# Kernel tuning notes

Measured on AMD Instinct MI355X. Metric: run time of the kernel, lower is better.

The kernel has to match this reference:

```python
import jax, jax.numpy as jnp
import numpy as np

N = 50000      # nodes
E = 600000     # edges (avg degree 12)
IN = 128       # in_feat
HID = IN // 2  # 64
OUT = 128      # out_feat (must equal in_feat, see msg_linear)

# NOTE: the torch source uses nn.LeakyReLU(True): the positional arg is
# negative_slope, so slope == 1.0 (identity). We reproduce that faithfully.
NEG_SLOPE = 1.0

def leaky(v):
    return jnp.where(v >= 0, v, NEG_SLOPE * v)

def _linear_params(key, fan_in, fan_out):
    kw, kb = jax.random.split(key)
    bound = 1.0 / np.sqrt(fan_in)
    W = jax.random.uniform(kw, (fan_in, fan_out), jnp.float32, -bound, bound)
    b = jax.random.uniform(kb, (fan_out,), jnp.float32, -bound, bound)
    return W, b

def setup_inputs() -> dict:
    key = jax.random.key(0)
    ks = jax.random.split(key, 10)
    x = jax.random.normal(ks[0], (N, IN), jnp.float32)
    e = jax.random.normal(ks[1], (E, IN), jnp.float32)
    src = jax.random.randint(ks[2], (E,), 0, N, jnp.int64)
    dst = jax.random.randint(ks[3], (E,), 0, N, jnp.int64)
    W_nl1, b_nl1 = _linear_params(ks[4], IN, HID)    # node_linear1
    W_el, b_el = _linear_params(ks[5], IN, HID)      # edge_linear
    W1, b1 = _linear_params(ks[6], HID, HID)         # node_mlp layer 1
    W2, b2 = _linear_params(ks[7], HID, OUT)         # node_mlp layer 2
    W_nl2, b_nl2 = _linear_params(ks[8], IN, HID)    # node_linear2
    km, ke = jax.random.split(ks[9])
    W_ml, b_ml = _linear_params(km, IN, HID)         # msg_linear (in_feat==out_feat)
    W_em, b_em = _linear_params(ke, HID, OUT)        # edge_mlp layer
    return dict(x=x, e=e, src=src, dst=dst,
                W_nl1=W_nl1, b_nl1=b_nl1, W_el=W_el, b_el=b_el,
                W1=W1, b1=b1, W2=W2, b2=b2,
                W_nl2=W_nl2, b_nl2=b_nl2, W_ml=W_ml, b_ml=b_ml,
                W_em=W_em, b_em=b_em)

def reference(x, e, src, dst,
              W_nl1, b_nl1, W_el, b_el,
              W1, b1, W2, b2,
              W_nl2, b_nl2, W_ml, b_ml,
              W_em, b_em):
    # apply_edges: e' = node_mlp(node_linear1(x[src]) + edge_linear(e))
    z = x[src] @ W_nl1 + b_nl1 + e @ W_el + b_el            # [E, HID]
    e_new = leaky(leaky(z) @ W1 + b1) @ W2 + b2             # [E, OUT]
    # update_all(copy_e, sum): scatter-sum edge messages to destination nodes
    msg = jax.ops.segment_sum(e_new, dst, num_segments=N)   # [N, OUT]
    # x' = edge_mlp(node_linear2(x) + msg_linear(msg))
    h = leaky(x @ W_nl2 + b_nl2 + msg @ W_ml + b_ml)        # [N, HID]
    return h @ W_em + b_em                                  # [N, OUT]
```

## Files before the change

kernel.cpp:

```cpp
#include <hip/hip_runtime.h>

#define N_NODES 50000
#define N_EDGES 600000

#define WF_XS   0
#define WF_ES   6400000
#define WI_CNT   12800000
#define WI_OFF   12850000
#define WI_CUR   12900000
#define WI_BSUM  12950000
#define WI_BOFF  12950256
#define WI_EPAIR 12950512
#define WF_U    14160000
#define WF_V    14168192
#define WF_G    14184576
#define WF_P    14192768
#define WF_Q    14209152
#define WF_C1   14225536
#define WF_BE   14241920
#define WF_R    14242048
#define WF_C2   14242176

#define NBLK_SCAN 196

__global__ void pre1_kernel(const float* __restrict__ W1, const float* __restrict__ W2,
                            const float* __restrict__ b1, const float* __restrict__ b2,
                            const float* __restrict__ W_ml, const float* __restrict__ W_em,
                            const float* __restrict__ W_nl2, const float* __restrict__ b_nl2,
                            const float* __restrict__ b_ml, const float* __restrict__ b_em,
                            float* __restrict__ U, float* __restrict__ V,
                            float* __restrict__ C1, float* __restrict__ be,
                            float* __restrict__ c2) {
    int idx = blockIdx.x * 256 + threadIdx.x;
    if (idx < 8192) {
        int i = idx >> 7, j = idx & 127;
        float s = 0.f;
        for (int k = 0; k < 64; ++k) s += W1[i*64+k] * W2[k*128+j];
        U[idx] = s;
    } else if (idx < 24576) {
        int t = idx - 8192; int i = t >> 7, j = t & 127;
        float s = 0.f;
        for (int k = 0; k < 64; ++k) s += W_ml[i*64+k] * W_em[k*128+j];
        V[t] = s;
    } else if (idx < 40960) {
        int t = idx - 24576; int i = t >> 7, j = t & 127;
        float s = 0.f;
        for (int k = 0; k < 64; ++k) s += W_nl2[i*64+k] * W_em[k*128+j];
        C1[t] = s;
    } else if (idx < 41088) {
        int j = idx - 40960;
        float s = b2[j];
        for (int k = 0; k < 64; ++k) s += b1[k] * W2[k*128+j];
        be[j] = s;
    } else if (idx < 41216) {
        int j = idx - 41088;
        float s = b_em[j];
        for (int k = 0; k < 64; ++k) s += (b_nl2[k] + b_ml[k]) * W_em[k*128+j];
        c2[j] = s;
    }
}

__global__ void pre2_kernel(const float* __restrict__ U, const float* __restrict__ V,
                            float* __restrict__ G) {
    int idx = blockIdx.x * 256 + threadIdx.x;
    if (idx >= 8192) return;
    int i = idx >> 7, j = idx & 127;
    float s = 0.f;
    for (int k = 0; k < 128; ++k) s += U[i*128+k] * V[k*128+j];
    G[idx] = s;
}

__global__ void pre3_kernel(const float* __restrict__ W_nl1, const float* __restrict__ W_el,
                            const float* __restrict__ b_nl1, const float* __restrict__ b_el,
                            const float* __restrict__ G, const float* __restrict__ V,
                            const float* __restrict__ be,
                            float* __restrict__ P, float* __restrict__ Q,
                            float* __restrict__ r) {
    int idx = blockIdx.x * 256 + threadIdx.x;
    if (idx < 16384) {
        int i = idx >> 7, j = idx & 127;
        float s = 0.f;
        for (int k = 0; k < 64; ++k) s += W_nl1[i*64+k] * G[k*128+j];
        P[idx] = s;
    } else if (idx < 32768) {
        int t = idx - 16384; int i = t >> 7, j = t & 127;
        float s = 0.f;
        for (int k = 0; k < 64; ++k) s += W_el[i*64+k] * G[k*128+j];
        Q[t] = s;
    } else if (idx < 32896) {
        int j = idx - 32768;
        float s = 0.f;
        for (int k = 0; k < 64; ++k)  s += (b_nl1[k] + b_el[k]) * G[k*128+j];
        for (int k = 0; k < 128; ++k) s += be[k] * V[k*128+j];
        r[j] = s;
    }
}

__global__ __launch_bounds__(256) void zero_kernel(int* __restrict__ cnt) {
    int i = blockIdx.x * 256 + threadIdx.x;
    if (i < N_NODES) cnt[i] = 0;
}

__global__ __launch_bounds__(256) void hist_kernel(const int* __restrict__ dst,
                                                   int* __restrict__ cnt) {
    int e = blockIdx.x * 256 + threadIdx.x;
    if (e < N_EDGES) atomicAdd(&cnt[dst[e]], 1);
}

__global__ __launch_bounds__(256) void scan_a_kernel(const int* __restrict__ cnt,
                                                     int* __restrict__ bsum) {
    __shared__ int s[256];
    int i = blockIdx.x * 256 + threadIdx.x;
    int v = (i < N_NODES) ? cnt[i] : 0;
    s[threadIdx.x] = v;
    __syncthreads();
    for (int d = 128; d > 0; d >>= 1) {
        if (threadIdx.x < d) s[threadIdx.x] += s[threadIdx.x + d];
        __syncthreads();
    }
    if (threadIdx.x == 0) bsum[blockIdx.x] = s[0];
}

__global__ __launch_bounds__(256) void scan_b_kernel(const int* __restrict__ bsum,
                                                     int* __restrict__ boff) {
    __shared__ int s[256];
    int t = threadIdx.x;
    int v = (t < NBLK_SCAN) ? bsum[t] : 0;
    s[t] = v;
    __syncthreads();
    for (int d = 1; d < 256; d <<= 1) {
        int tv = (t >= d) ? s[t - d] : 0;
        __syncthreads();
        s[t] += tv;
        __syncthreads();
    }
    if (t < NBLK_SCAN) boff[t] = s[t] - v;
}

__global__ __launch_bounds__(256) void scan_c_kernel(const int* __restrict__ cnt,
                                                     const int* __restrict__ boff,
                                                     int* __restrict__ offs,
                                                     int* __restrict__ cursor) {
    __shared__ int s[256];
    int i = blockIdx.x * 256 + threadIdx.x;
    int t = threadIdx.x;
    int v = (i < N_NODES) ? cnt[i] : 0;
    s[t] = v;
    __syncthreads();
    for (int d = 1; d < 256; d <<= 1) {
        int tv = (t >= d) ? s[t - d] : 0;
        __syncthreads();
        s[t] += tv;
        __syncthreads();
    }
    if (i < N_NODES) {
        int ex = s[t] - v + boff[blockIdx.x];
        offs[i] = ex;
        cursor[i] = ex;
    }
}

__global__ __launch_bounds__(256) void fill_kernel(const int* __restrict__ dst,
                                                   const int* __restrict__ src,
                                                   int* __restrict__ cursor,
                                                   int2* __restrict__ epair) {
    int e = blockIdx.x * 256 + threadIdx.x;
    if (e < N_EDGES) {
        int pos = atomicAdd(&cursor[dst[e]], 1);
        epair[pos] = make_int2(e, src[e]);
    }
}

__global__ __launch_bounds__(256) void gather_kernel(
        const float* __restrict__ x, const float* __restrict__ ef,
        const int* __restrict__ cnt, const int* __restrict__ offs,
        const int2* __restrict__ epair,
        float* __restrict__ xs, float* __restrict__ es) {
    int n    = (int)((blockIdx.x * 256 + threadIdx.x) >> 6);
    int lane = threadIdx.x & 63;
    if (n >= N_NODES) return;
    int off = offs[n], deg = cnt[n];
    int col2 = lane * 2;
    float ax0 = 0.f, ax1 = 0.f, ae0 = 0.f, ae1 = 0.f;
    for (int c0 = 0; c0 < deg; c0 += 64) {
        int j = c0 + lane;
        int2 p = make_int2(0, 0);
        if (j < deg) p = epair[off + j];
        int m = deg - c0; if (m > 64) m = 64;
        int j2 = 0;
        for (; j2 + 8 <= m; j2 += 8) {
            float2 xv[8], ev[8];
            #pragma unroll
            for (int u = 0; u < 8; ++u) {
                int e_ = __shfl(p.x, j2 + u);
                int s_ = __shfl(p.y, j2 + u);
                xv[u] = *(const float2*)(x  + (size_t)s_ * 128 + col2);
                ev[u] = *(const float2*)(ef + (size_t)e_ * 128 + col2);
            }
            #pragma unroll
            for (int u = 0; u < 8; ++u) {
                ax0 += xv[u].x; ax1 += xv[u].y;
                ae0 += ev[u].x; ae1 += ev[u].y;
            }
        }
        for (; j2 < m; ++j2) {
            int e_ = __shfl(p.x, j2);
            int s_ = __shfl(p.y, j2);
            float2 xv = *(const float2*)(x  + (size_t)s_ * 128 + col2);
            float2 ev = *(const float2*)(ef + (size_t)e_ * 128 + col2);
            ax0 += xv.x; ax1 += xv.y;
            ae0 += ev.x; ae1 += ev.y;
        }
    }
    *(float2*)(xs + (size_t)n * 128 + col2) = make_float2(ax0, ax1);
    *(float2*)(es + (size_t)n * 128 + col2) = make_float2(ae0, ae1);
}

__global__ __launch_bounds__(256) void out_gemm_kernel(
        const float* __restrict__ x, const float* __restrict__ xs,
        const float* __restrict__ es, const int* __restrict__ cnt,
        const float* __restrict__ C1, const float* __restrict__ P,
        const float* __restrict__ Q,
        const float* __restrict__ rvec, const float* __restrict__ c2,
        float* __restrict__ out) {
    __shared__ float As[32][133];
    __shared__ float Ws[32][128];
    int base = blockIdx.x * 128;
    int t = threadIdx.x;
    int cg = t & 15, rg = t >> 4;
    int c0 = cg * 8, r0 = rg * 8;

    float4 rva = *(const float4*)&rvec[c0];
    float4 rvb = *(const float4*)&rvec[c0 + 4];
    float4 cva = *(const float4*)&c2[c0];
    float4 cvb = *(const float4*)&c2[c0 + 4];
    float acc[8][8];
    #pragma unroll
    for (int i = 0; i < 8; ++i) {
        int n = base + r0 + i;
        float dg = (n < N_NODES) ? (float)cnt[n] : 0.f;
        acc[i][0] = cva.x + dg * rva.x;  acc[i][1] = cva.y + dg * rva.y;
        acc[i][2] = cva.z + dg * rva.z;  acc[i][3] = cva.w + dg * rva.w;
        acc[i][4] = cvb.x + dg * rvb.x;  acc[i][5] = cvb.y + dg * rvb.y;
        acc[i][6] = cvb.z + dg * rvb.z;  acc[i][7] = cvb.w + dg * rvb.w;
    }

    int arow0 = t >> 3;
    int akq   = t & 7;

    #pragma unroll
    for (int m = 0; m < 3; ++m) {
        const float* __restrict__ S = (m == 0) ? x : (m == 1) ? xs : es;
        const float* __restrict__ W = (m == 0) ? C1 : (m == 1) ? P : Q;
        for (int k0 = 0; k0 < 128; k0 += 32) {
            __syncthreads();
            #pragma unroll
            for (int i = 0; i < 4; ++i) {
                int row = arow0 + i * 32;
                int n = base + row;
                float4 v = make_float4(0.f, 0.f, 0.f, 0.f);
                if (n < N_NODES)
                    v = *(const float4*)&S[(size_t)n * 128 + k0 + akq * 4];
                As[akq * 4 + 0][row] = v.x;
                As[akq * 4 + 1][row] = v.y;
                As[akq * 4 + 2][row] = v.z;
                As[akq * 4 + 3][row] = v.w;
            }
            #pragma unroll
            for (int i = 0; i < 4; ++i) {
                int idx = t + i * 256;
                int row = idx >> 5, q4 = idx & 31;
                *(float4*)&Ws[row][q4 * 4] =
                    *(const float4*)&W[(size_t)(k0 + row) * 128 + q4 * 4];
            }
            __syncthreads();
            #pragma unroll 8
            for (int k = 0; k < 32; ++k) {
                float a[8], w[8];
                *(float4*)&a[0] = *(const float4*)&As[k][r0];
                *(float4*)&a[4] = *(const float4*)&As[k][r0 + 4];
                *(float4*)&w[0] = *(const float4*)&Ws[k][c0];
                *(float4*)&w[4] = *(const float4*)&Ws[k][c0 + 4];
                #pragma unroll
                for (int i = 0; i < 8; ++i)
                    #pragma unroll
                    for (int jj = 0; jj < 8; ++jj)
                        acc[i][jj] += a[i] * w[jj];
            }
        }
    }

    #pragma unroll
    for (int i = 0; i < 8; ++i) {
        int n = base + r0 + i;
        if (n < N_NODES) {
            *(float4*)&out[(size_t)n * 128 + c0]     = *(float4*)&acc[i][0];
            *(float4*)&out[(size_t)n * 128 + c0 + 4] = *(float4*)&acc[i][4];
        }
    }
}

extern "C" void kernel_launch(void* const* d_in, const int* in_sizes, int n_in,
                              void* d_out, int out_size, void* d_ws, size_t ws_size,
                              hipStream_t stream) {
    const float* x     = (const float*)d_in[0];
    const float* ef    = (const float*)d_in[1];
    const int*   src   = (const int*)d_in[2];
    const int*   dst   = (const int*)d_in[3];
    const float* W_nl1 = (const float*)d_in[4];
    const float* b_nl1 = (const float*)d_in[5];
    const float* W_el  = (const float*)d_in[6];
    const float* b_el  = (const float*)d_in[7];
    const float* W1    = (const float*)d_in[8];
    const float* b1    = (const float*)d_in[9];
    const float* W2    = (const float*)d_in[10];
    const float* b2    = (const float*)d_in[11];
    const float* W_nl2 = (const float*)d_in[12];
    const float* b_nl2 = (const float*)d_in[13];
    const float* W_ml  = (const float*)d_in[14];
    const float* b_ml  = (const float*)d_in[15];
    const float* W_em  = (const float*)d_in[16];
    const float* b_em  = (const float*)d_in[17];

    int*   wsI = (int*)d_ws;
    float* wsF = (float*)d_ws;
    float* xs     = wsF + WF_XS;
    float* es     = wsF + WF_ES;
    int*   cnt    = wsI + WI_CNT;
    int*   offs   = wsI + WI_OFF;
    int*   cursor = wsI + WI_CUR;
    int*   bsum   = wsI + WI_BSUM;
    int*   boff   = wsI + WI_BOFF;
    int2*  epair  = (int2*)(wsI + WI_EPAIR);
    float* U  = wsF + WF_U;
    float* V  = wsF + WF_V;
    float* G  = wsF + WF_G;
    float* P  = wsF + WF_P;
    float* Q  = wsF + WF_Q;
    float* C1 = wsF + WF_C1;
    float* be = wsF + WF_BE;
    float* r  = wsF + WF_R;
    float* c2 = wsF + WF_C2;

    zero_kernel<<<NBLK_SCAN, 256, 0, stream>>>(cnt);

    pre1_kernel<<<(41216 + 255) / 256, 256, 0, stream>>>(
        W1, W2, b1, b2, W_ml, W_em, W_nl2, b_nl2, b_ml, b_em, U, V, C1, be, c2);
    pre2_kernel<<<8192 / 256, 256, 0, stream>>>(U, V, G);
    pre3_kernel<<<(32896 + 255) / 256, 256, 0, stream>>>(
        W_nl1, W_el, b_nl1, b_el, G, V, be, P, Q, r);

    hist_kernel<<<(N_EDGES + 255) / 256, 256, 0, stream>>>(dst, cnt);
    scan_a_kernel<<<NBLK_SCAN, 256, 0, stream>>>(cnt, bsum);
    scan_b_kernel<<<1, 256, 0, stream>>>(bsum, boff);
    scan_c_kernel<<<NBLK_SCAN, 256, 0, stream>>>(cnt, boff, offs, cursor);
    fill_kernel<<<(N_EDGES + 255) / 256, 256, 0, stream>>>(dst, src, cursor, epair);

    gather_kernel<<<(N_NODES + 3) / 4, 256, 0, stream>>>(
        x, ef, cnt, offs, epair, xs, es);

    out_gemm_kernel<<<(N_NODES + 127) / 128, 256, 0, stream>>>(
        x, xs, es, cnt, C1, P, Q, r, c2, (float*)d_out);
}
```

Before: 285.3 us.

## Factor output GEMM through 64-wide hidden space to halve FLOPs

Instead of folding W_em into 128-wide combined weights, the node-side GEMM now projects x, xs and es onto a 64-wide hidden vector u, then a second GEMM multiplies by W_em and adds degree-scaled bias terms. Precomputed weight products are reassociated to stay in the 64-wide space. This cuts the multiply-add count of the output stage roughly in half, at the cost of writing and rereading an N×64 intermediate and one more kernel launch.

```diff
diff --git a/kernel.cpp b/kernel.cpp
--- a/kernel.cpp
+++ b/kernel.cpp
@@ -5,94 +5,95 @@
 
 #define WF_XS   0
 #define WF_ES   6400000
-#define WI_CNT   12800000
-#define WI_OFF   12850000
-#define WI_CUR   12900000
-#define WI_BSUM  12950000
-#define WI_BOFF  12950256
-#define WI_EPAIR 12950512
-#define WF_U    14160000
-#define WF_V    14168192
-#define WF_G    14184576
-#define WF_P    14192768
-#define WF_Q    14209152
-#define WF_C1   14225536
-#define WF_BE   14241920
-#define WF_R    14242048
-#define WF_C2   14242176
+#define WF_UN   12800000
+#define WI_CNT   16000000
+#define WI_OFF   16050000
+#define WI_CUR   16100000
+#define WI_BSUM  16150000
+#define WI_BOFF  16150256
+#define WI_EPAIR 16150512
+#define WF_T2   17350528
+#define WF_BEG  17354624
+#define WF_RH   17354752
+#define WF_K1   17354816
+#define WF_WA   17358912
+#define WF_R    17383488
+#define WF_C2   17383616
 
 #define NBLK_SCAN 196
 
-__global__ void pre1_kernel(const float* __restrict__ W1, const float* __restrict__ W2,
-                            const float* __restrict__ b1, const float* __restrict__ b2,
-                            const float* __restrict__ W_ml, const float* __restrict__ W_em,
-                            const float* __restrict__ W_nl2, const float* __restrict__ b_nl2,
-                            const float* __restrict__ b_ml, const float* __restrict__ b_em,
-                            float* __restrict__ U, float* __restrict__ V,
-                            float* __restrict__ C1, float* __restrict__ be,
-                            float* __restrict__ c2) {
+__global__ __launch_bounds__(256) void pre_t2_kernel(
+        const float* __restrict__ W2, const float* __restrict__ W_ml,
+        const float* __restrict__ b1, const float* __restrict__ b2,
+        float* __restrict__ T2, float* __restrict__ be_g) {
+    int idx = blockIdx.x * 256 + threadIdx.x;
+    if (idx < 4096) {
+        int i = idx >> 6, j = idx & 63;
+        float s = 0.f;
+        for (int k = 0; k < 128; ++k) s += W2[i*128+k] * W_ml[k*64+j];
+        T2[idx] = s;
+    } else if (idx < 4224) {
+        int j = idx - 4096;
+        float s = b2[j];
+        for (int k = 0; k < 64; ++k) s += b1[k] * W2[k*128+j];
+        be_g[j] = s;
+    }
+}
+
+__global__ __launch_bounds__(256) void pre_k1_kernel(
+        const float* __restrict__ W1, const float* __restrict__ T2,
+        float* __restrict__ K1) {
+    int idx = blockIdx.x * 256 + threadIdx.x;
+    if (idx >= 4096) return;
+    int i = idx >> 6, j = idx & 63;
+    float s = 0.f;
+    for (int k = 0; k < 64; ++k) s += W1[i*64+k] * T2[k*64+j];
+    K1[idx] = s;
+}
+
+__global__ __launch_bounds__(256) void pre_wa_kernel(
+        const float* __restrict__ W_nl1, const float* __restrict__ W_el,
+        const float* __restrict__ W_nl2, const float* __restrict__ K1,
+        const float* __restrict__ b_nl1, const float* __restrict__ b_el,
+        const float* __restrict__ be_g, const float* __restrict__ W_ml,
+        float* __restrict__ WA, float* __restrict__ rh_g) {
     int idx = blockIdx.x * 256 + threadIdx.x;
     if (idx < 8192) {
-        int i = idx >> 7, j = idx & 127;
+        WA[idx] = W_nl2[idx];
+    } else if (idx < 16384) {
+        int p = idx - 8192; int i = p >> 6, j = p & 63;
         float s = 0.f;
-        for (int k = 0; k < 64; ++k) s += W1[i*64+k] * W2[k*128+j];
-        U[idx] = s;
+        for (int k = 0; k < 64; ++k) s += W_nl1[i*64+k] * K1[k*64+j];
+        WA[idx] = s;
     } else if (idx < 24576) {
-        int t = idx - 8192; int i = t >> 7, j = t & 127;
+        int p = idx - 16384; int i = p >> 6, j = p & 63;
         float s = 0.f;
-        for (int k = 0; k < 64; ++k) s += W_ml[i*64+k] * W_em[k*128+j];
-        V[t] = s;
-    } else if (idx < 40960) {
-        int t = idx - 24576; int i = t >> 7, j = t & 127;
+        for (int k = 0; k < 64; ++k) s += W_el[i*64+k] * K1[k*64+j];
+        WA[idx] = s;
+    } else if (idx < 24640) {
+        int t = idx - 24576;
         float s = 0.f;
-        for (int k = 0; k < 64; ++k) s += W_nl2[i*64+k] * W_em[k*128+j];
-        C1[t] = s;
-    } else if (idx < 41088) {
-        int j = idx - 40960;
-        float s = b2[j];
-        for (int k = 0; k < 64; ++k) s += b1[k] * W2[k*128+j];
-        be[j] = s;
-    } else if (idx < 41216) {
-        int j = idx - 41088;
+        for (int k = 0; k < 64; ++k)  s += (b_nl1[k] + b_el[k]) * K1[k*64+t];
+        for (int k = 0; k < 128; ++k) s += be_g[k] * W_ml[k*64+t];
+        rh_g[t] = s;
+    }
+}
+
+__global__ __launch_bounds__(256) void pre_rc_kernel(
+        const float* __restrict__ rh_g, const float* __restrict__ W_em,
+        const float* __restrict__ b_nl2, const float* __restrict__ b_ml,
+        const float* __restrict__ b_em,
+        float* __restrict__ r, float* __restrict__ c2) {
+    int idx = threadIdx.x;
+    if (idx < 128) {
+        float s = 0.f;
+        for (int k = 0; k < 64; ++k) s += rh_g[k] * W_em[k*128+idx];
+        r[idx] = s;
+    } else {
+        int j = idx - 128;
         float s = b_em[j];
         for (int k = 0; k < 64; ++k) s += (b_nl2[k] + b_ml[k]) * W_em[k*128+j];
         c2[j] = s;
-    }
-}
-
-__global__ void pre2_kernel(const float* __restrict__ U, const float* __restrict__ V,
-                            float* __restrict__ G) {
-    int idx = blockIdx.x * 256 + threadIdx.x;
-    if (idx >= 8192) return;
-    int i = idx >> 7, j = idx & 127;
-    float s = 0.f;
-    for (int k = 0; k < 128; ++k) s += U[i*128+k] * V[k*128+j];
-    G[idx] = s;
-}
-
-__global__ void pre3_kernel(const float* __restrict__ W_nl1, const float* __restrict__ W_el,
-                            const float* __restrict__ b_nl1, const float* __restrict__ b_el,
-                            const float* __restrict__ G, const float* __restrict__ V,
-                            const float* __restrict__ be,
-                            float* __restrict__ P, float* __restrict__ Q,
-                            float* __restrict__ r) {
-    int idx = blockIdx.x * 256 + threadIdx.x;
-    if (idx < 16384) {
-        int i = idx >> 7, j = idx & 127;
-        float s = 0.f;
-        for (int k = 0; k < 64; ++k) s += W_nl1[i*64+k] * G[k*128+j];
-        P[idx] = s;
-    } else if (idx < 32768) {
-        int t = idx - 16384; int i = t >> 7, j = t & 127;
-        float s = 0.f;
-        for (int k = 0; k < 64; ++k) s += W_el[i*64+k] * G[k*128+j];
-        Q[t] = s;
-    } else if (idx < 32896) {
-        int j = idx - 32768;
-        float s = 0.f;
-        for (int k = 0; k < 64; ++k)  s += (b_nl1[k] + b_el[k]) * G[k*128+j];
-        for (int k = 0; k < 128; ++k) s += be[k] * V[k*128+j];
-        r[j] = s;
     }
 }
 
@@ -216,34 +217,22 @@
     *(float2*)(es + (size_t)n * 128 + col2) = make_float2(ae0, ae1);
 }
 
-__global__ __launch_bounds__(256) void out_gemm_kernel(
+__global__ __launch_bounds__(256) void gemm1_kernel(
         const float* __restrict__ x, const float* __restrict__ xs,
-        const float* __restrict__ es, const int* __restrict__ cnt,
-        const float* __restrict__ C1, const float* __restrict__ P,
-        const float* __restrict__ Q,
-        const float* __restrict__ rvec, const float* __restrict__ c2,
-        float* __restrict__ out) {
+        const float* __restrict__ es, const float* __restrict__ WA,
+        float* __restrict__ u) {
     __shared__ float As[32][133];
-    __shared__ float Ws[32][128];
+    __shared__ float Ws[32][64];
     int base = blockIdx.x * 128;
     int t = threadIdx.x;
     int cg = t & 15, rg = t >> 4;
-    int c0 = cg * 8, r0 = rg * 8;
-
-    float4 rva = *(const float4*)&rvec[c0];
-    float4 rvb = *(const float4*)&rvec[c0 + 4];
-    float4 cva = *(const float4*)&c2[c0];
-    float4 cvb = *(const float4*)&c2[c0 + 4];
-    float acc[8][8];
-    #pragma unroll
-    for (int i = 0; i < 8; ++i) {
-        int n = base + r0 + i;
-        float dg = (n < N_NODES) ? (float)cnt[n] : 0.f;
-        acc[i][0] = cva.x + dg * rva.x;  acc[i][1] = cva.y + dg * rva.y;
-        acc[i][2] = cva.z + dg * rva.z;  acc[i][3] = cva.w + dg * rva.w;
-        acc[i][4] = cvb.x + dg * rvb.x;  acc[i][5] = cvb.y + dg * rvb.y;
-        acc[i][6] = cvb.z + dg * rvb.z;  acc[i][7] = cvb.w + dg * rvb.w;
-    }
+    int c0 = cg * 4, r0 = rg * 8;
+
+    float acc[8][4];
+    #pragma unroll
+    for (int i = 0; i < 8; ++i)
+        #pragma unroll
+        for (int j = 0; j < 4; ++j) acc[i][j] = 0.f;
 
     int arow0 = t >> 3;
     int akq   = t & 7;
@@ -251,7 +240,6 @@
     #pragma unroll
     for (int m = 0; m < 3; ++m) {
         const float* __restrict__ S = (m == 0) ? x : (m == 1) ? xs : es;
-        const float* __restrict__ W = (m == 0) ? C1 : (m == 1) ? P : Q;
         for (int k0 = 0; k0 < 128; k0 += 32) {
             __syncthreads();
             #pragma unroll
@@ -267,31 +255,100 @@
                 As[akq * 4 + 3][row] = v.w;
             }
             #pragma unroll
-            for (int i = 0; i < 4; ++i) {
+            for (int i = 0; i < 2; ++i) {
                 int idx = t + i * 256;
-                int row = idx >> 5, q4 = idx & 31;
+                int row = idx >> 4, q4 = idx & 15;
                 *(float4*)&Ws[row][q4 * 4] =
-                    *(const float4*)&W[(size_t)(k0 + row) * 128 + q4 * 4];
+                    *(const float4*)&WA[(size_t)(m * 128 + k0 + row) * 64 + q4 * 4];
             }
             __syncthreads();
             #pragma unroll 8
             for (int k = 0; k < 32; ++k) {
-                float a[8], w[8];
+                float a[8];
                 *(float4*)&a[0] = *(const float4*)&As[k][r0];
                 *(float4*)&a[4] = *(const float4*)&As[k][r0 + 4];
-                *(float4*)&w[0] = *(const float4*)&Ws[k][c0];
-                *(float4*)&w[4] = *(const float4*)&Ws[k][c0 + 4];
+                float4 w = *(const float4*)&Ws[k][c0];
                 #pragma unroll
-                for (int i = 0; i < 8; ++i)
-                    #pragma unroll
-                    for (int jj = 0; jj < 8; ++jj)
-                        acc[i][jj] += a[i] * w[jj];
+                for (int i = 0; i < 8; ++i) {
+                    acc[i][0] += a[i] * w.x;
+                    acc[i][1] += a[i] * w.y;
+                    acc[i][2] += a[i] * w.z;
+                    acc[i][3] += a[i] * w.w;
+                }
             }
         }
     }
 
     #pragma unroll
     for (int i = 0; i < 8; ++i) {
+        int n = base + r0 + i;
+        if (n < N_NODES)
+            *(float4*)&u[(size_t)n * 64 + c0] = *(float4*)&acc[i][0];
+    }
+}
+
+__global__ __launch_bounds__(256) void gemm2_kernel(
+        const float* __restrict__ u, const int* __restrict__ cnt,
+        const float* __restrict__ W_em,
+        const float* __restrict__ rvec, const float* __restrict__ c2,
+        float* __restrict__ out) {
+    __shared__ float UsT[64][69];
+    __shared__ float Wem[64][128];
+    int base = blockIdx.x * 64;
+    int t = threadIdx.x;
+    int cg = t & 15, rg = t >> 4;
+    int c0 = cg * 8, r0 = rg * 4;
+
+    #pragma unroll
+    for (int i = 0; i < 4; ++i) {
+        int idx = t + i * 256;
+        int row = idx >> 4, kq = idx & 15;
+        int n = base + row;
+        float4 v = make_float4(0.f, 0.f, 0.f, 0.f);
+        if (n < N_NODES) v = *(const float4*)&u[(size_t)n * 64 + kq * 4];
+        UsT[kq * 4 + 0][row] = v.x;
+        UsT[kq * 4 + 1][row] = v.y;
+        UsT[kq * 4 + 2][row] = v.z;
+        UsT[kq * 4 + 3][row] = v.w;
+    }
+    #pragma unroll
+    for (int i = 0; i < 8; ++i) {
+        int idx = t + i * 256;
+        int row = idx >> 5, q4 = idx & 31;
+        *(float4*)&Wem[row][q4 * 4] = *(const float4*)&W_em[(size_t)row * 128 + q4 * 4];
+    }
+
+    float4 rva = *(const float4*)&rvec[c0];
+    float4 rvb = *(const float4*)&rvec[c0 + 4];
+    float4 cva = *(const float4*)&c2[c0];
+    float4 cvb = *(const float4*)&c2[c0 + 4];
+    float acc[4][8];
+    #pragma unroll
+    for (int i = 0; i < 4; ++i) {
+        int n = base + r0 + i;
+        float dg = (n < N_NODES) ? (float)cnt[n] : 0.f;
+        acc[i][0] = cva.x + dg * rva.x;  acc[i][1] = cva.y + dg * rva.y;
+        acc[i][2] = cva.z + dg * rva.z;  acc[i][3] = cva.w + dg * rva.w;
+        acc[i][4] = cvb.x + dg * rvb.x;  acc[i][5] = cvb.y + dg * rvb.y;
+        acc[i][6] = cvb.z + dg * rvb.z;  acc[i][7] = cvb.w + dg * rvb.w;
+    }
+    __syncthreads();
+
+    #pragma unroll 8
+    for (int k = 0; k < 64; ++k) {
+        float a[4], w[8];
+        *(float4*)&a[0] = *(const float4*)&UsT[k][r0];
+        *(float4*)&w[0] = *(const float4*)&Wem[k][c0];
+        *(float4*)&w[4] = *(const float4*)&Wem[k][c0 + 4];
+        #pragma unroll
+        for (int i = 0; i < 4; ++i)
+            #pragma unroll
+            for (int j = 0; j < 8; ++j)
+                acc[i][j] += a[i] * w[j];
+    }
+
+    #pragma unroll
+    for (int i = 0; i < 4; ++i) {
         int n = base + r0 + i;
         if (n < N_NODES) {
             *(float4*)&out[(size_t)n * 128 + c0]     = *(float4*)&acc[i][0];
@@ -326,30 +383,28 @@
     float* wsF = (float*)d_ws;
     float* xs     = wsF + WF_XS;
     float* es     = wsF + WF_ES;
+    float* uN     = wsF + WF_UN;
     int*   cnt    = wsI + WI_CNT;
     int*   offs   = wsI + WI_OFF;
     int*   cursor = wsI + WI_CUR;
     int*   bsum   = wsI + WI_BSUM;
     int*   boff   = wsI + WI_BOFF;
     int2*  epair  = (int2*)(wsI + WI_EPAIR);
-    float* U  = wsF + WF_U;
-    float* V  = wsF + WF_V;
-    float* G  = wsF + WF_G;
-    float* P  = wsF + WF_P;
-    float* Q  = wsF + WF_Q;
-    float* C1 = wsF + WF_C1;
-    float* be = wsF + WF_BE;
-    float* r  = wsF + WF_R;
-    float* c2 = wsF + WF_C2;
+    float* T2   = wsF + WF_T2;
+    float* be_g = wsF + WF_BEG;
+    float* rh_g = wsF + WF_RH;
+    float* K1   = wsF + WF_K1;
+    float* WA   = wsF + WF_WA;
+    float* r    = wsF + WF_R;
+    float* c2   = wsF + WF_C2;
+
+    pre_t2_kernel<<<17, 256, 0, stream>>>(W2, W_ml, b1, b2, T2, be_g);
+    pre_k1_kernel<<<16, 256, 0, stream>>>(W1, T2, K1);
+    pre_wa_kernel<<<97, 256, 0, stream>>>(W_nl1, W_el, W_nl2, K1,
+                                          b_nl1, b_el, be_g, W_ml, WA, rh_g);
+    pre_rc_kernel<<<1, 256, 0, stream>>>(rh_g, W_em, b_nl2, b_ml, b_em, r, c2);
 
     zero_kernel<<<NBLK_SCAN, 256, 0, stream>>>(cnt);
-
-    pre1_kernel<<<(41216 + 255) / 256, 256, 0, stream>>>(
-        W1, W2, b1, b2, W_ml, W_em, W_nl2, b_nl2, b_ml, b_em, U, V, C1, be, c2);
-    pre2_kernel<<<8192 / 256, 256, 0, stream>>>(U, V, G);
-    pre3_kernel<<<(32896 + 255) / 256, 256, 0, stream>>>(
-        W_nl1, W_el, b_nl1, b_el, G, V, be, P, Q, r);
-
     hist_kernel<<<(N_EDGES + 255) / 256, 256, 0, stream>>>(dst, cnt);
     scan_a_kernel<<<NBLK_SCAN, 256, 0, stream>>>(cnt, bsum);
     scan_b_kernel<<<1, 256, 0, stream>>>(bsum, boff);
@@ -359,6 +414,7 @@
     gather_kernel<<<(N_NODES + 3) / 4, 256, 0, stream>>>(
         x, ef, cnt, offs, epair, xs, es);
 
-    out_gemm_kernel<<<(N_NODES + 127) / 128, 256, 0, stream>>>(
-        x, xs, es, cnt, C1, P, Q, r, c2, (float*)d_out);
-}
+    gemm1_kernel<<<(N_NODES + 127) / 128, 256, 0, stream>>>(x, xs, es, WA, uN);
+    gemm2_kernel<<<(N_NODES + 63) / 64, 256, 0, stream>>>(
+        uN, cnt, W_em, r, c2, (float*)d_out);
+}
```

New measurement: 278.9 us. 2.2% less time.
